# Optimization experiments

Measured on AMD Instinct MI355X. Metric: run time of the kernel, lower is better.

The kernel has to match this reference:

```python
import jax, jax.numpy as jnp
import numpy as np

N_NODES = 100000


def setup_inputs() -> dict:
    key = jax.random.key(0)
    k1, k2, k3, k4, k5, k6 = jax.random.split(key, 6)
    n_edges = 1600000
    in_f, out_f = 64, 64
    x = jax.random.normal(k1, (N_NODES, in_f), dtype=jnp.float32)
    edge_row = jax.random.randint(k2, (n_edges,), 0, N_NODES, dtype=jnp.int32)
    edge_col = jax.random.randint(k3, (n_edges,), 0, N_NODES, dtype=jnp.int32)
    edge_val = jax.random.uniform(k4, (n_edges,), dtype=jnp.float32)
    stdv = 1.0 / np.sqrt(out_f)
    weight = jax.random.uniform(k5, (in_f, out_f), dtype=jnp.float32, minval=-stdv, maxval=stdv)
    bias = jax.random.uniform(k6, (out_f,), dtype=jnp.float32, minval=-stdv, maxval=stdv)
    return {"x": x, "edge_row": edge_row, "edge_col": edge_col,
            "edge_val": edge_val, "weight": weight, "bias": bias}


def reference(x, edge_row, edge_col, edge_val, weight, bias):
    # spmm: support[i] = sum_{e: row[e]==i} val[e] * x[col[e]]
    msgs = edge_val[:, None] * x[edge_col]              # [E, in_f]
    support = jax.ops.segment_sum(msgs, edge_row, num_segments=N_NODES)  # [N, in_f]
    out = support @ weight + bias                       # [N, out_f]
    # row-wise L2 normalize (no eps, matching torch.norm division)
    norm = jnp.linalg.norm(out, axis=1, keepdims=True)  # [N, 1]
    return out / norm
```

## Files before the change

### kernel.cpp

```cpp
#include <hip/hip_runtime.h>

#define N_NODES 100000
#define FDIM 64
#define BROWS 64
#define NBUCK ((N_NODES + BROWS - 1) / BROWS)
#define EDGES_PER_BLK 8192
#define BCAP 1536

#define WS_BBASE_OFF (656u * 1024u)
#define WS_BTOT_OFF  (672u * 1024u)
#define WS_CV_OFF    (1024u * 1024u)
#define WS_XH_OFF    (14u * 1024u * 1024u)

__device__ __forceinline__ unsigned short f2bf(float f) {
    unsigned int u = __float_as_uint(f);
    return (unsigned short)((u + 0x7FFFu + ((u >> 16) & 1u)) >> 16);
}
__device__ __forceinline__ float bf2f(unsigned short h) {
    return __uint_as_float((unsigned int)h << 16);
}

__global__ __launch_bounds__(256) void spmm_atomic(
    const float* __restrict__ x, const int* __restrict__ erow,
    const int* __restrict__ ecol, const float* __restrict__ eval,
    float* __restrict__ out, int n_edges)
{
    int tid = blockIdx.x * 256 + threadIdx.x;
    int e = tid >> 4, l = tid & 15;
    if (e >= n_edges) return;
    int row = erow[e], col = ecol[e];
    float v = eval[e];
    const float4 xv = *reinterpret_cast<const float4*>(x + (size_t)col * FDIM + l * 4);
    float* dst = out + (size_t)row * FDIM + l * 4;
    unsafeAtomicAdd(dst + 0, v * xv.x);
    unsafeAtomicAdd(dst + 1, v * xv.y);
    unsafeAtomicAdd(dst + 2, v * xv.z);
    unsafeAtomicAdd(dst + 3, v * xv.w);
}

__global__ __launch_bounds__(256) void gemm_xw(
    const float* __restrict__ x, const float* __restrict__ W,
    unsigned short* __restrict__ yh)
{
    __shared__ float4 Wl[64][16];
    __shared__ float  s[4][4][68];

    const int t = threadIdx.x;
    for (int i = t; i < 64 * 16; i += 256)
        ((float4*)Wl)[i] = ((const float4*)W)[i];

    const int wid  = t >> 6;
    const int lane = t & 63;
    const int sub  = lane >> 4;
    const int l    = lane & 15;
    const long base = (long)blockIdx.x * 16 + wid * 4;

    float4 sv = *reinterpret_cast<const float4*>(x + base * FDIM + lane * 4);
    *reinterpret_cast<float4*>(&s[wid][lane >> 4][(lane & 15) * 4]) = sv;
    __syncthreads();

    float4 acc = {0.f, 0.f, 0.f, 0.f};
    const float* srow = s[wid][sub];
    #pragma unroll
    for (int k = 0; k < FDIM; ++k) {
        const float a = srow[k];
        const float4 w = Wl[k][l];
        acc.x += a * w.x; acc.y += a * w.y; acc.z += a * w.z; acc.w += a * w.w;
    }
    ushort4 h;
    h.x = f2bf(acc.x); h.y = f2bf(acc.y); h.z = f2bf(acc.z); h.w = f2bf(acc.w);
    *reinterpret_cast<ushort4*>(yh + (size_t)(base + sub) * FDIM + l * 4) = h;
}

__global__ __launch_bounds__(1024) void count_blocks(
    const int* __restrict__ erow, unsigned short* __restrict__ cnts,
    int n_edges, int nblk)
{
    __shared__ int cnt[NBUCK];
    const int blk = blockIdx.x, t = threadIdx.x;
    for (int i = t; i < NBUCK; i += 1024) cnt[i] = 0;
    __syncthreads();
    const int beg = blk * EDGES_PER_BLK;
    const int end = min(beg + EDGES_PER_BLK, n_edges);
    for (int i = beg + t; i < end; i += 1024)
        atomicAdd(&cnt[erow[i] >> 6], 1);
    __syncthreads();
    for (int b = t; b < NBUCK; b += 1024)
        cnts[b * nblk + blk] = (unsigned short)cnt[b];
}

__global__ __launch_bounds__(256) void scan_within_bucket(
    unsigned short* __restrict__ cnts, int* __restrict__ btot, int nblk)
{
    __shared__ int ssum[256];
    const int b = blockIdx.x, t = threadIdx.x;
    const int c = (t < nblk) ? (int)cnts[b * nblk + t] : 0;
    ssum[t] = c;
    __syncthreads();
    for (int off = 1; off < 256; off <<= 1) {
        int v = (t >= off) ? ssum[t - off] : 0;
        __syncthreads();
        ssum[t] += v;
        __syncthreads();
    }
    if (t < nblk) cnts[b * nblk + t] = (unsigned short)(ssum[t] - c);
    if (t == 255) btot[b] = ssum[255];
}

__global__ __launch_bounds__(1024) void scan_btot(
    const int* __restrict__ btot, int* __restrict__ bbase, int n_edges)
{
    __shared__ int ssum[1024];
    const int t = threadIdx.x;
    const int i0 = 2 * t, i1 = 2 * t + 1;
    const int v0 = (i0 < NBUCK) ? btot[i0] : 0;
    const int v1 = (i1 < NBUCK) ? btot[i1] : 0;
    const int s = v0 + v1;
    ssum[t] = s;
    __syncthreads();
    for (int off = 1; off < 1024; off <<= 1) {
        int v = (t >= off) ? ssum[t - off] : 0;
        __syncthreads();
        ssum[t] += v;
        __syncthreads();
    }
    int base = ssum[t] - s;
    if (i0 < NBUCK) bbase[i0] = base;
    if (i1 < NBUCK) bbase[i1] = base + v0;
    if (t == 0) bbase[NBUCK] = n_edges;
}

__global__ __launch_bounds__(1024) void bin_pass2(
    const int* __restrict__ erow, const int* __restrict__ ecol,
    const float* __restrict__ eval, const unsigned short* __restrict__ cnts,
    const int* __restrict__ bbase, int2* __restrict__ cvbin,
    int n_edges, int nblk)
{
    __shared__ int cur[NBUCK];
    const int blk = blockIdx.x, t = threadIdx.x;
    for (int b = t; b < NBUCK; b += 1024)
        cur[b] = bbase[b] + (int)cnts[b * nblk + blk];
    __syncthreads();
    const int beg = blk * EDGES_PER_BLK;
    const int end = min(beg + EDGES_PER_BLK, n_edges);
    for (int i = beg + t; i < end; i += 1024) {
        int r = erow[i];
        int b = r >> 6;
        int pos = atomicAdd(&cur[b], 1);
        cvbin[pos] = make_int2(ecol[i] | ((r & 63) << 20), __float_as_int(eval[i]));
    }
}

__global__ __launch_bounds__(256) void sort_spmm(
    const int* __restrict__ bbase, const int2* __restrict__ cvbin,
    const unsigned short* __restrict__ yh, const float* __restrict__ bias,
    float* __restrict__ out)
{
    __shared__ int2 se[BCAP];
    __shared__ int  hcnt[BROWS];
    __shared__ int  scn[BROWS];
    __shared__ int  rowbeg[BROWS];
    __shared__ int  cur[BROWS];

    const int b = blockIdx.x, t = threadIdx.x;
    const int beg = bbase[b];
    const int end = bbase[b + 1];
    const int n = end - beg;
    const bool fits = (n <= BCAP);

    if (t < BROWS) hcnt[t] = 0;
    __syncthreads();

    if (fits) {
        for (int i = t; i < n; i += 256)
            atomicAdd(&hcnt[(cvbin[beg + i].x >> 20) & 63], 1);
        __syncthreads();
        if (t < BROWS) scn[t] = hcnt[t];
        __syncthreads();
        for (int off = 1; off < BROWS; off <<= 1) {
            int v = (t < BROWS && t >= off) ? scn[t - off] : 0;
            __syncthreads();
            if (t < BROWS) scn[t] += v;
            __syncthreads();
        }
        if (t < BROWS) { rowbeg[t] = scn[t] - hcnt[t]; cur[t] = scn[t] - hcnt[t]; }
        __syncthreads();
        for (int i = t; i < n; i += 256) {
            int2 e = cvbin[beg + i];
            int pos = atomicAdd(&cur[(e.x >> 20) & 63], 1);
            se[pos] = e;
        }
        __syncthreads();
    }

    const int sg = t >> 4, l = t & 15;
    #pragma unroll
    for (int rr = 0; rr < 4; ++rr) {
        const int r = sg + 16 * rr;
        const int row = b * BROWS + r;
        float4 acc = {0.f, 0.f, 0.f, 0.f};

        if (fits) {
            const int rb = rowbeg[r];
            const int re = rb + hcnt[r];
            int it = rb;
            for (; it + 3 < re; it += 4) {
                const int2 ea = se[it];
                const int2 eb = se[it + 1];
                const int2 ec = se[it + 2];
                const int2 ed = se[it + 3];
                const ushort4 xa = *reinterpret_cast<const ushort4*>(yh + (size_t)(ea.x & 0xFFFFF) * FDIM + l * 4);
                const ushort4 xb = *reinterpret_cast<const ushort4*>(yh + (size_t)(eb.x & 0xFFFFF) * FDIM + l * 4);
                const ushort4 xc = *reinterpret_cast<const ushort4*>(yh + (size_t)(ec.x & 0xFFFFF) * FDIM + l * 4);
                const ushort4 xd = *reinterpret_cast<const ushort4*>(yh + (size_t)(ed.x & 0xFFFFF) * FDIM + l * 4);
                const float va = __int_as_float(ea.y);
                const float vb = __int_as_float(eb.y);
                const float vc = __int_as_float(ec.y);
                const float vd = __int_as_float(ed.y);
                acc.x += va * bf2f(xa.x); acc.y += va * bf2f(xa.y); acc.z += va * bf2f(xa.z); acc.w += va * bf2f(xa.w);
                acc.x += vb * bf2f(xb.x); acc.y += vb * bf2f(xb.y); acc.z += vb * bf2f(xb.z); acc.w += vb * bf2f(xb.w);
                acc.x += vc * bf2f(xc.x); acc.y += vc * bf2f(xc.y); acc.z += vc * bf2f(xc.z); acc.w += vc * bf2f(xc.w);
                acc.x += vd * bf2f(xd.x); acc.y += vd * bf2f(xd.y); acc.z += vd * bf2f(xd.z); acc.w += vd * bf2f(xd.w);
            }
            for (; it < re; ++it) {
                const int2 e = se[it];
                const float v = __int_as_float(e.y);
                const ushort4 xv = *reinterpret_cast<const ushort4*>(yh + (size_t)(e.x & 0xFFFFF) * FDIM + l * 4);
                acc.x += v * bf2f(xv.x); acc.y += v * bf2f(xv.y); acc.z += v * bf2f(xv.z); acc.w += v * bf2f(xv.w);
            }
        } else {
            for (int i = beg; i < end; ++i) {
                const int2 e = cvbin[i];
                if (((e.x >> 20) & 63) == r) {
                    const float v = __int_as_float(e.y);
                    const ushort4 xv = *reinterpret_cast<const ushort4*>(yh + (size_t)(e.x & 0xFFFFF) * FDIM + l * 4);
                    acc.x += v * bf2f(xv.x); acc.y += v * bf2f(xv.y); acc.z += v * bf2f(xv.z); acc.w += v * bf2f(xv.w);
                }
            }
        }

        const float4 bv = *reinterpret_cast<const float4*>(bias + l * 4);
        acc.x += bv.x; acc.y += bv.y; acc.z += bv.z; acc.w += bv.w;

        float p = acc.x * acc.x + acc.y * acc.y + acc.z * acc.z + acc.w * acc.w;
        #pragma unroll
        for (int off = 1; off < 16; off <<= 1)
            p += __shfl_xor(p, off);
        const float inv = 1.0f / sqrtf(p);
        acc.x *= inv; acc.y *= inv; acc.z *= inv; acc.w *= inv;

        if (row < N_NODES)
            *reinterpret_cast<float4*>(out + (size_t)row * FDIM + l * 4) = acc;
    }
}

__global__ __launch_bounds__(256) void gemm_norm(
    float* __restrict__ io, const float* __restrict__ W,
    const float* __restrict__ bias)
{
    __shared__ float4 Wl[64][16];
    __shared__ float4 bl[16];
    __shared__ float  s[4][4][68];

    const int t = threadIdx.x;
    for (int i = t; i < 64 * 16; i += 256)
        ((float4*)Wl)[i] = ((const float4*)W)[i];
    if (t < 16) bl[t] = ((const float4*)bias)[t];

    const int wid  = t >> 6;
    const int lane = t & 63;
    const int sub  = lane >> 4;
    const int l    = lane & 15;
    const long base = (long)blockIdx.x * 16 + wid * 4;

    float4 sv = *reinterpret_cast<const float4*>(io + base * FDIM + lane * 4);
    *reinterpret_cast<float4*>(&s[wid][lane >> 4][(lane & 15) * 4]) = sv;
    __syncthreads();

    float4 acc = {0.f, 0.f, 0.f, 0.f};
    const float* srow = s[wid][sub];
    #pragma unroll
    for (int k = 0; k < FDIM; ++k) {
        const float a = srow[k];
        const float4 w = Wl[k][l];
        acc.x += a * w.x; acc.y += a * w.y; acc.z += a * w.z; acc.w += a * w.w;
    }
    const float4 b = bl[l];
    acc.x += b.x; acc.y += b.y; acc.z += b.z; acc.w += b.w;

    float p = acc.x*acc.x + acc.y*acc.y + acc.z*acc.z + acc.w*acc.w;
    #pragma unroll
    for (int off = 1; off < 16; off <<= 1)
        p += __shfl_xor(p, off);
    const float inv = 1.0f / sqrtf(p);
    acc.x *= inv; acc.y *= inv; acc.z *= inv; acc.w *= inv;

    *reinterpret_cast<float4*>(io + (base + sub) * FDIM + l * 4) = acc;
}

extern "C" void kernel_launch(void* const* d_in, const int* in_sizes, int n_in,
                              void* d_out, int out_size, void* d_ws, size_t ws_size,
                              hipStream_t stream) {
    const float* x    = (const float*)d_in[0];
    const int*   erow = (const int*)d_in[1];
    const int*   ecol = (const int*)d_in[2];
    const float* eval = (const float*)d_in[3];
    const float* W    = (const float*)d_in[4];
    const float* bias = (const float*)d_in[5];
    float* out = (float*)d_out;
    const int n_edges = in_sizes[1];

    const int nblk = (n_edges + EDGES_PER_BLK - 1) / EDGES_PER_BLK;
    const size_t need_bf16 = (size_t)WS_XH_OFF + (size_t)N_NODES * FDIM * sizeof(short);
    const bool cnts_fit =
        (size_t)NBUCK * nblk * sizeof(unsigned short) <= WS_BBASE_OFF
        && nblk <= 256 && EDGES_PER_BLK <= 65535;

    if (ws_size >= need_bf16 && cnts_fit) {
        unsigned short* cnts = (unsigned short*)d_ws;
        int*  bbase  = (int*)((char*)d_ws + WS_BBASE_OFF);
        int*  btot   = (int*)((char*)d_ws + WS_BTOT_OFF);
        int2* cvbin  = (int2*)((char*)d_ws + WS_CV_OFF);
        unsigned short* yh = (unsigned short*)((char*)d_ws + WS_XH_OFF);

        gemm_xw<<<N_NODES / 16, 256, 0, stream>>>(x, W, yh);
        count_blocks<<<nblk, 1024, 0, stream>>>(erow, cnts, n_edges, nblk);
        scan_within_bucket<<<NBUCK, 256, 0, stream>>>(cnts, btot, nblk);
        scan_btot<<<1, 1024, 0, stream>>>(btot, bbase, n_edges);
        bin_pass2<<<nblk, 1024, 0, stream>>>(erow, ecol, eval, cnts, bbase, cvbin,
                                             n_edges, nblk);
        sort_spmm<<<NBUCK, 256, 0, stream>>>(bbase, cvbin, yh, bias, out);
    } else {
        hipMemsetAsync(out, 0, (size_t)N_NODES * FDIM * sizeof(float), stream);
        long threads = (long)n_edges * 16;
        spmm_atomic<<<(int)((threads + 255) / 256), 256, 0, stream>>>(
            x, erow, ecol, eval, out, n_edges);
        gemm_norm<<<N_NODES / 16, 256, 0, stream>>>(out, W, bias);
    }
}
```

Before: 92.77 us.

## Fuse GEMM with edge counting and merge the two scans into one launch

The x@W GEMM and the per-block bucket counting now run as two block ranges of a single kernel, and bucket totals are accumulated with global atomics instead of being produced by the within-bucket scan. The within-bucket scan and the bucket-base scan then run in one launch, with one extra block doing the totals scan. This removes two kernel launches and the serial dependency between them. In exchange it adds a memset, global atomics on btot, and a much larger shared-memory footprint for the GEMM blocks, since every block reserves the count array.

```diff
diff --git a/kernel.cpp b/kernel.cpp
--- a/kernel.cpp
+++ b/kernel.cpp
@@ -6,6 +6,8 @@
 #define NBUCK ((N_NODES + BROWS - 1) / BROWS)
 #define EDGES_PER_BLK 8192
 #define BCAP 1536
+#define GEMM_BLOCKS ((N_NODES + 63) / 64)
+#define SCAN_C ((NBUCK + 255) / 256)
 
 #define WS_BBASE_OFF (656u * 1024u)
 #define WS_BTOT_OFF  (672u * 1024u)
@@ -38,96 +40,106 @@
     unsafeAtomicAdd(dst + 3, v * xv.w);
 }
 
-__global__ __launch_bounds__(256) void gemm_xw(
+__global__ __launch_bounds__(1024) void gemm_count(
     const float* __restrict__ x, const float* __restrict__ W,
-    unsigned short* __restrict__ yh)
+    unsigned short* __restrict__ yh,
+    const int* __restrict__ erow, unsigned short* __restrict__ cnts,
+    int* __restrict__ btot, int n_edges, int nblk)
 {
     __shared__ float4 Wl[64][16];
-    __shared__ float  s[4][4][68];
+    __shared__ float  s[16][4][68];
+    __shared__ int    cnt[NBUCK];
 
     const int t = threadIdx.x;
-    for (int i = t; i < 64 * 16; i += 256)
-        ((float4*)Wl)[i] = ((const float4*)W)[i];
-
-    const int wid  = t >> 6;
-    const int lane = t & 63;
-    const int sub  = lane >> 4;
-    const int l    = lane & 15;
-    const long base = (long)blockIdx.x * 16 + wid * 4;
-
-    float4 sv = *reinterpret_cast<const float4*>(x + base * FDIM + lane * 4);
-    *reinterpret_cast<float4*>(&s[wid][lane >> 4][(lane & 15) * 4]) = sv;
-    __syncthreads();
-
-    float4 acc = {0.f, 0.f, 0.f, 0.f};
-    const float* srow = s[wid][sub];
-    #pragma unroll
-    for (int k = 0; k < FDIM; ++k) {
-        const float a = srow[k];
-        const float4 w = Wl[k][l];
-        acc.x += a * w.x; acc.y += a * w.y; acc.z += a * w.z; acc.w += a * w.w;
-    }
-    ushort4 h;
-    h.x = f2bf(acc.x); h.y = f2bf(acc.y); h.z = f2bf(acc.z); h.w = f2bf(acc.w);
-    *reinterpret_cast<ushort4*>(yh + (size_t)(base + sub) * FDIM + l * 4) = h;
-}
-
-__global__ __launch_bounds__(1024) void count_blocks(
-    const int* __restrict__ erow, unsigned short* __restrict__ cnts,
-    int n_edges, int nblk)
-{
-    __shared__ int cnt[NBUCK];
-    const int blk = blockIdx.x, t = threadIdx.x;
-    for (int i = t; i < NBUCK; i += 1024) cnt[i] = 0;
-    __syncthreads();
-    const int beg = blk * EDGES_PER_BLK;
-    const int end = min(beg + EDGES_PER_BLK, n_edges);
-    for (int i = beg + t; i < end; i += 1024)
-        atomicAdd(&cnt[erow[i] >> 6], 1);
-    __syncthreads();
-    for (int b = t; b < NBUCK; b += 1024)
-        cnts[b * nblk + blk] = (unsigned short)cnt[b];
-}
-
-__global__ __launch_bounds__(256) void scan_within_bucket(
-    unsigned short* __restrict__ cnts, int* __restrict__ btot, int nblk)
+    if ((int)blockIdx.x < GEMM_BLOCKS) {
+        ((float4*)Wl)[t] = ((const float4*)W)[t];
+
+        const int wid  = t >> 6;
+        const int lane = t & 63;
+        const int sub  = lane >> 4;
+        const int l    = lane & 15;
+        const long base = (long)blockIdx.x * 64 + wid * 4;
+        const bool valid = (base + 3 < N_NODES);
+
+        float4 sv = {0.f, 0.f, 0.f, 0.f};
+        if (valid) sv = *reinterpret_cast<const float4*>(x + base * FDIM + lane * 4);
+        *reinterpret_cast<float4*>(&s[wid][lane >> 4][(lane & 15) * 4]) = sv;
+        __syncthreads();
+
+        if (valid) {
+            float4 acc = {0.f, 0.f, 0.f, 0.f};
+            const float* srow = s[wid][sub];
+            #pragma unroll
+            for (int k = 0; k < FDIM; ++k) {
+                const float a = srow[k];
+                const float4 w = Wl[k][l];
+                acc.x += a * w.x; acc.y += a * w.y; acc.z += a * w.z; acc.w += a * w.w;
+            }
+            ushort4 h;
+            h.x = f2bf(acc.x); h.y = f2bf(acc.y); h.z = f2bf(acc.z); h.w = f2bf(acc.w);
+            *reinterpret_cast<ushort4*>(yh + (size_t)(base + sub) * FDIM + l * 4) = h;
+        }
+    } else {
+        const int blk = (int)blockIdx.x - GEMM_BLOCKS;
+        for (int i = t; i < NBUCK; i += 1024) cnt[i] = 0;
+        __syncthreads();
+        const int beg = blk * EDGES_PER_BLK;
+        const int end = min(beg + EDGES_PER_BLK, n_edges);
+        for (int i = beg + t; i < end; i += 1024)
+            atomicAdd(&cnt[erow[i] >> 6], 1);
+        __syncthreads();
+        for (int b = t; b < NBUCK; b += 1024) {
+            const int c = cnt[b];
+            cnts[b * nblk + blk] = (unsigned short)c;
+            if (c) atomicAdd(&btot[b], c);
+        }
+    }
+}
+
+__global__ __launch_bounds__(256) void scan_bb(
+    unsigned short* __restrict__ cnts, const int* __restrict__ btot,
+    int* __restrict__ bbase, int n_edges, int nblk)
 {
     __shared__ int ssum[256];
     const int b = blockIdx.x, t = threadIdx.x;
-    const int c = (t < nblk) ? (int)cnts[b * nblk + t] : 0;
-    ssum[t] = c;
-    __syncthreads();
-    for (int off = 1; off < 256; off <<= 1) {
-        int v = (t >= off) ? ssum[t - off] : 0;
-        __syncthreads();
-        ssum[t] += v;
-        __syncthreads();
-    }
-    if (t < nblk) cnts[b * nblk + t] = (unsigned short)(ssum[t] - c);
-    if (t == 255) btot[b] = ssum[255];
-}
-
-__global__ __launch_bounds__(1024) void scan_btot(
-    const int* __restrict__ btot, int* __restrict__ bbase, int n_edges)
-{
-    __shared__ int ssum[1024];
-    const int t = threadIdx.x;
-    const int i0 = 2 * t, i1 = 2 * t + 1;
-    const int v0 = (i0 < NBUCK) ? btot[i0] : 0;
-    const int v1 = (i1 < NBUCK) ? btot[i1] : 0;
-    const int s = v0 + v1;
-    ssum[t] = s;
-    __syncthreads();
-    for (int off = 1; off < 1024; off <<= 1) {
-        int v = (t >= off) ? ssum[t - off] : 0;
-        __syncthreads();
-        ssum[t] += v;
-        __syncthreads();
-    }
-    int base = ssum[t] - s;
-    if (i0 < NBUCK) bbase[i0] = base;
-    if (i1 < NBUCK) bbase[i1] = base + v0;
-    if (t == 0) bbase[NBUCK] = n_edges;
+
+    if (b < NBUCK) {
+        const int c = (t < nblk) ? (int)cnts[b * nblk + t] : 0;
+        ssum[t] = c;
+        __syncthreads();
+        for (int off = 1; off < 256; off <<= 1) {
+            int v = (t >= off) ? ssum[t - off] : 0;
+            __syncthreads();
+            ssum[t] += v;
+            __syncthreads();
+        }
+        if (t < nblk) cnts[b * nblk + t] = (unsigned short)(ssum[t] - c);
+    } else {
+        int v[SCAN_C];
+        int s = 0;
+        #pragma unroll
+        for (int k = 0; k < SCAN_C; ++k) {
+            const int idx = t * SCAN_C + k;
+            v[k] = (idx < NBUCK) ? btot[idx] : 0;
+            s += v[k];
+        }
+        ssum[t] = s;
+        __syncthreads();
+        for (int off = 1; off < 256; off <<= 1) {
+            int vv = (t >= off) ? ssum[t - off] : 0;
+            __syncthreads();
+            ssum[t] += vv;
+            __syncthreads();
+        }
+        int base = ssum[t] - s;
+        #pragma unroll
+        for (int k = 0; k < SCAN_C; ++k) {
+            const int idx = t * SCAN_C + k;
+            if (idx < NBUCK) bbase[idx] = base;
+            base += v[k];
+        }
+        if (t == 0) bbase[NBUCK] = n_edges;
+    }
 }
 
 __global__ __launch_bounds__(1024) void bin_pass2(
@@ -323,10 +335,10 @@
         int2* cvbin  = (int2*)((char*)d_ws + WS_CV_OFF);
         unsigned short* yh = (unsigned short*)((char*)d_ws + WS_XH_OFF);
 
-        gemm_xw<<<N_NODES / 16, 256, 0, stream>>>(x, W, yh);
-        count_blocks<<<nblk, 1024, 0, stream>>>(erow, cnts, n_edges, nblk);
-        scan_within_bucket<<<NBUCK, 256, 0, stream>>>(cnts, btot, nblk);
-        scan_btot<<<1, 1024, 0, stream>>>(btot, bbase, n_edges);
+        hipMemsetAsync(btot, 0, NBUCK * sizeof(int), stream);
+        gemm_count<<<GEMM_BLOCKS + nblk, 1024, 0, stream>>>(
+            x, W, yh, erow, cnts, btot, n_edges, nblk);
+        scan_bb<<<NBUCK + 1, 256, 0, stream>>>(cnts, btot, bbase, n_edges, nblk);
         bin_pass2<<<nblk, 1024, 0, stream>>>(erow, ecol, eval, cnts, bbase, cvbin,
                                              n_edges, nblk);
         sort_spmm<<<NBUCK, 256, 0, stream>>>(bbase, cvbin, yh, bias, out);
```

After: 95.75 us. 3.2% more time.
